# Kernel tuning notes

Measured on AMD Instinct MI355X. Metric: run time of the kernel, lower is better.

The kernel has to match this reference:

```python
import jax, jax.numpy as jnp
import numpy as np

# Static video grid (F, H, W); S = F*H*W tokens.
F_FRAMES, H_GRID, W_GRID = 9, 16, 28
DIM, N_HEADS = 1536, 12
HEAD_DIM = DIM // N_HEADS          # 128
ROT = HEAD_DIM // 2                # 64 complex pairs
EPS = 1e-6


def setup_inputs() -> dict:
    key = jax.random.key(0)
    ks = jax.random.split(key, 12)
    S = F_FRAMES * H_GRID * W_GRID
    scale = 0.02
    inp = {
        "x": jax.random.normal(ks[0], (1, S, DIM), jnp.float32),
        "seq_lens": jnp.array([S], jnp.int32),
        "grid_sizes": jnp.array([[F_FRAMES, H_GRID, W_GRID]], jnp.int32),
        "freqs": jax.random.normal(ks[1], (1024, ROT), jnp.float32),  # rope angles
        "Wq": jax.random.normal(ks[2], (DIM, DIM), jnp.float32) * scale,
        "bq": jnp.zeros((DIM,), jnp.float32),
        "Wk": jax.random.normal(ks[3], (DIM, DIM), jnp.float32) * scale,
        "bk": jnp.zeros((DIM,), jnp.float32),
        "Wv": jax.random.normal(ks[4], (DIM, DIM), jnp.float32) * scale,
        "bv": jnp.zeros((DIM,), jnp.float32),
        "Wo": jax.random.normal(ks[5], (DIM, DIM), jnp.float32) * scale,
        "bo": jnp.zeros((DIM,), jnp.float32),
        "gq": jnp.ones((DIM,), jnp.float32),
        "gk": jnp.ones((DIM,), jnp.float32),
    }
    return inp


def _rms_norm(h, g):
    # WanRMSNorm: h * rsqrt(mean(h^2) + eps) * weight
    var = jnp.mean(jnp.square(h), axis=-1, keepdims=True)
    return h * jax.lax.rsqrt(var + EPS) * g


def _rope_angles(freqs):
    # Split channel dim into temporal / height / width parts.
    c = ROT
    t_dim = c - 2 * (c // 3)  # 22
    s1 = c // 3               # 21
    temporal, height, width = freqs[:, :t_dim], freqs[:, t_dim:t_dim + s1], freqs[:, t_dim + s1:]
    t_ang = jnp.repeat(temporal[:F_FRAMES], H_GRID * W_GRID, axis=0)         # [S, 22]
    h_ang = jnp.tile(jnp.repeat(height[:H_GRID], W_GRID, axis=0), (F_FRAMES, 1))  # [S, 21]
    w_ang = jnp.tile(jnp.tile(width[:W_GRID], (H_GRID, 1)), (F_FRAMES, 1))        # [S, 21]
    return jnp.concatenate([t_ang, h_ang, w_ang], axis=-1)  # [S, c]


def _rope_apply(x, ang):
    # x: [B, S, n, d] viewed as complex pairs [B, S, n, d/2, 2]
    b, s, n, d = x.shape
    xp = x.reshape(b, s, n, d // 2, 2)
    xr, xi = xp[..., 0], xp[..., 1]
    cos = jnp.cos(ang)[None, :, None, :]
    sin = jnp.sin(ang)[None, :, None, :]
    out_r = xr * cos - xi * sin
    out_i = xr * sin + xi * cos
    return jnp.stack([out_r, out_i], axis=-1).reshape(b, s, n, d)


def reference(x, seq_lens, grid_sizes, freqs, Wq, bq, Wk, bk, Wv, bv, Wo, bo, gq, gk):
    b, s, _ = x.shape
    n, d = N_HEADS, HEAD_DIM
    q = _rms_norm(x @ Wq + bq, gq).reshape(b, s, n, d)
    k = _rms_norm(x @ Wk + bk, gk).reshape(b, s, n, d)
    v = (x @ Wv + bv).reshape(b, s, n, d)

    ang = _rope_angles(freqs)  # [S, d/2]
    rq = _rope_apply(q, ang)
    rk = _rope_apply(k, ang)

    # Causal frame-block mask: query in frame i attends to kv in frames <= i.
    frame_idx = jnp.arange(s) // (H_GRID * W_GRID)
    mask = frame_idx[None, :] <= frame_idx[:, None]  # [S_q, S_k]

    scale = 1.0 / jnp.sqrt(jnp.asarray(d, x.dtype))
    scores = jnp.einsum("bqnd,bknd->bnqk", rq, rk) * scale
    scores = jnp.where(mask[None, None], scores, jnp.asarray(-1e30, scores.dtype))
    probs = jax.nn.softmax(scores, axis=-1)
    attn = jnp.einsum("bnqk,bknd->bqnd", probs, v).reshape(b, s, n * d)
    return attn @ Wo + bo
```

## Files before the change

kernel.cpp:

```cpp
#include <hip/hip_runtime.h>
#include <stdint.h>

typedef unsigned short u16;
typedef unsigned int u32;
typedef __attribute__((ext_vector_type(8))) short bf16x8;
typedef __attribute__((ext_vector_type(4))) float f32x4;

#define S_LEN 4032
#define S_PAD 4096
#define DIMC  1536
#define HD    128
#define FRAME 448

static const size_t OFF_FLAG  = 0;
static const size_t OFF_CANON = 256;
static const size_t OFF_XB    = 524288;
static const size_t OFF_WT    = OFF_XB  + 12582912;
static const size_t OFF_WOT   = OFF_WT  + 14155776;
static const size_t OFF_YQ    = OFF_WOT + 4718592;
static const size_t OFF_YK    = OFF_YQ  + 12582912;
static const size_t OFF_VT    = OFF_YK  + 12582912;
static const size_t OFF_QH    = OFF_VT  + 12582912;
static const size_t OFF_KH    = OFF_QH  + 12386304;
static const size_t OFF_AT    = OFF_KH  + 12386304;
static const size_t WS_NEED   = OFF_AT  + 12582912;

#define C_BQ 0
#define C_BO 4608
#define C_GQ 6144
#define C_GK 7680
#define C_FR 9216
#define C_TOT 74752

__device__ __forceinline__ u16 f2bf(float f) {
  union { float f; u32 u; } v; v.f = f;
  u32 u = v.u;
  u32 r = (u + 0x7fffu + ((u >> 16) & 1u)) >> 16;
  return (u16)r;
}
__device__ __forceinline__ float bf2f(u16 h) {
  union { float f; u32 u; } v; v.u = ((u32)h) << 16;
  return v.f;
}

__device__ __forceinline__ void gld_lds16(const void* g, void* l) {
  __builtin_amdgcn_global_load_lds(
      (const __attribute__((address_space(1))) void*)(uintptr_t)g,
      (__attribute__((address_space(3))) void*)(u32)(uintptr_t)l,
      16, 0, 0);
}

__device__ __forceinline__ f32x4 mfma16(bf16x8 a, bf16x8 b, f32x4 c) {
  return __builtin_amdgcn_mfma_f32_16x16x32_bf16(a, b, c, 0, 0, 0);
}

__global__ void detect_dtype(const u16* __restrict__ x, int* __restrict__ flag) {
  __shared__ int cnt;
  if (threadIdx.x == 0) cnt = 0;
  __syncthreads();
  int e = (x[2 * threadIdx.x] >> 7) & 0xff;
  if (e > 150) atomicAdd(&cnt, 1);
  __syncthreads();
  if (threadIdx.x == 0) *flag = (cnt >= 8) ? 1 : 0;
}

__global__ void prep_small(const void* bq, const void* bk, const void* bv, const void* bo,
                           const void* gq, const void* gk, const void* fr,
                           float* __restrict__ canon, const int* __restrict__ flagp) {
  int fl = *flagp;
  for (int i = blockIdx.x * 256 + threadIdx.x; i < C_TOT; i += gridDim.x * 256) {
    const void* src; int j;
    if      (i < 1536) { src = bq; j = i; }
    else if (i < 3072) { src = bk; j = i - 1536; }
    else if (i < 4608) { src = bv; j = i - 3072; }
    else if (i < 6144) { src = bo; j = i - 4608; }
    else if (i < 7680) { src = gq; j = i - 6144; }
    else if (i < 9216) { src = gk; j = i - 7680; }
    else               { src = fr; j = i - 9216; }
    canon[i] = fl ? ((const float*)src)[j] : bf2f(((const u16*)src)[j]);
  }
}

__global__ void convert_x(const void* __restrict__ xin, u16* __restrict__ xb,
                          const int* __restrict__ flagp) {
  int fl = *flagp;
  int i = blockIdx.x * 256 + threadIdx.x;
  if (i >= (S_PAD * DIMC) / 8) return;
  size_t base = (size_t)i * 8;
  int row = (int)(base / DIMC);
  union { u16 h[8]; uint4 v; } u;
  if (row < S_LEN) {
    if (fl) {
      const float* xf = (const float*)xin + base;
      #pragma unroll
      for (int j = 0; j < 8; j++) u.h[j] = f2bf(xf[j]);
    } else {
      const u16* xh = (const u16*)xin + base;
      #pragma unroll
      for (int j = 0; j < 8; j++) u.h[j] = xh[j];
    }
  } else {
    #pragma unroll
    for (int j = 0; j < 8; j++) u.h[j] = 0;
  }
  ((uint4*)xb)[i] = u.v;
}

__global__ void transpose_w(const void* Wq, const void* Wk, const void* Wv, const void* Wo,
                            u16* __restrict__ wqkvt, u16* __restrict__ wot,
                            const int* __restrict__ flagp) {
  int fl = *flagp;
  int z = blockIdx.z;
  const void* W = (z == 0) ? Wq : (z == 1) ? Wk : (z == 2) ? Wv : Wo;
  u16* dst = (z < 3) ? (wqkvt + (size_t)z * DIMC * DIMC) : wot;
  __shared__ float tile[32][33];
  int tx = threadIdx.x, ty = threadIdx.y;
  int c = blockIdx.x * 32 + tx;
  #pragma unroll
  for (int i = 0; i < 4; i++) {
    int r = blockIdx.y * 32 + ty + i * 8;
    float v = fl ? ((const float*)W)[(size_t)r * DIMC + c]
                 : bf2f(((const u16*)W)[(size_t)r * DIMC + c]);
    tile[ty + i * 8][tx] = v;
  }
  __syncthreads();
  int k = blockIdx.y * 32 + tx;
  #pragma unroll
  for (int i = 0; i < 4; i++) {
    int n = blockIdx.x * 32 + ty + i * 8;
    dst[(size_t)n * DIMC + k] = f2bf(tile[tx][ty + i * 8]);
  }
}

template <int MODE, int NBN>
__launch_bounds__(256, 4)
__global__ void gemm_bt(const u16* __restrict__ A, const u16* __restrict__ Bt,
                        const float* __restrict__ canon,
                        u16* __restrict__ Yq, u16* __restrict__ Yk, u16* __restrict__ Vt,
                        void* __restrict__ Out, const int* __restrict__ flagp) {
  const int bid = blockIdx.x;
  const int panel = bid / (8 * NBN);
  const int rem = bid % (8 * NBN);
  const int bm0 = (panel * 8 + (rem % 8)) * 128;
  const int bn0 = (rem / 8) * 128;
  const int tid = threadIdx.x, wave = tid >> 6, lane = tid & 63;
  const int wm = wave >> 1, wn = wave & 1;
  const int l15 = lane & 15, l4 = lane >> 4;
  __shared__ u16 sA[128 * 64];
  __shared__ u16 sB[128 * 64];
  f32x4 acc[4][4];
  #pragma unroll
  for (int i = 0; i < 4; i++)
    #pragma unroll
    for (int j = 0; j < 4; j++) acc[i][j] = (f32x4){0.f, 0.f, 0.f, 0.f};

  const int swc = ((lane & 7) ^ (lane >> 3)) * 8;
  const u16* Ab = A  + (size_t)(bm0 + (lane >> 3)) * DIMC + swc;
  const u16* Bb = Bt + (size_t)(bn0 + (lane >> 3)) * DIMC + swc;

  for (int kt = 0; kt < DIMC; kt += 64) {
    __syncthreads();
    #pragma unroll
    for (int c = 0; c < 4; c++) {
      int g = wave * 4 + c;
      gld_lds16(Ab + (size_t)g * 8 * DIMC + kt, (char*)sA + g * 1024);
      gld_lds16(Bb + (size_t)g * 8 * DIMC + kt, (char*)sB + g * 1024);
    }
    __syncthreads();
    #pragma unroll
    for (int ks = 0; ks < 2; ks++) {
      bf16x8 av[4], bvv[4];
      #pragma unroll
      for (int mt = 0; mt < 4; mt++)
        av[mt]  = *(const bf16x8*)(sA + (wm * 64 + mt * 16 + l15) * 64 +
                                   (((ks * 4 + l4) ^ (l15 & 7)) * 8));
      #pragma unroll
      for (int nt = 0; nt < 4; nt++)
        bvv[nt] = *(const bf16x8*)(sB + (wn * 64 + nt * 16 + l15) * 64 +
                                   (((ks * 4 + l4) ^ (l15 & 7)) * 8));
      #pragma unroll
      for (int mt = 0; mt < 4; mt++)
        #pragma unroll
        for (int nt = 0; nt < 4; nt++)
          acc[mt][nt] = mfma16(av[mt], bvv[nt], acc[mt][nt]);
    }
  }

  const int gm0 = bm0 + wm * 64;
  const int gn0 = bn0 + wn * 64;
  if (MODE == 0) {
    #pragma unroll
    for (int nt = 0; nt < 4; nt++) {
      int gn = gn0 + nt * 16 + l15;
      float b = canon[C_BQ + gn];
      #pragma unroll
      for (int mt = 0; mt < 4; mt++) {
        int gm = gm0 + mt * 16 + l4 * 4;
        if (gn < 1536) {
          #pragma unroll
          for (int r = 0; r < 4; r++)
            Yq[(size_t)(gm + r) * DIMC + gn] = f2bf(acc[mt][nt][r] + b);
        } else if (gn < 3072) {
          int g2 = gn - 1536;
          #pragma unroll
          for (int r = 0; r < 4; r++)
            Yk[(size_t)(gm + r) * DIMC + g2] = f2bf(acc[mt][nt][r] + b);
        } else {
          int g2 = gn - 3072;
          u32 lo = (u32)f2bf(acc[mt][nt][0] + b) | ((u32)f2bf(acc[mt][nt][1] + b) << 16);
          u32 hi = (u32)f2bf(acc[mt][nt][2] + b) | ((u32)f2bf(acc[mt][nt][3] + b) << 16);
          uint2 pk; pk.x = lo; pk.y = hi;
          *(uint2*)(Vt + (size_t)g2 * S_PAD + gm) = pk;
        }
      }
    }
  } else {
    const int fl = *flagp;
    #pragma unroll
    for (int nt = 0; nt < 4; nt++) {
      int gn = gn0 + nt * 16 + l15;
      float b = canon[C_BO + gn];
      #pragma unroll
      for (int mt = 0; mt < 4; mt++) {
        int gm = gm0 + mt * 16 + l4 * 4;
        #pragma unroll
        for (int r = 0; r < 4; r++) {
          int gr = gm + r;
          if (gr < S_LEN) {
            float v = acc[mt][nt][r] + b;
            if (fl) ((float*)Out)[(size_t)gr * DIMC + gn] = v;
            else    ((u16*)Out)[(size_t)gr * DIMC + gn] = f2bf(v);
          }
        }
      }
    }
  }
}

__global__ void norm_rope(const u16* __restrict__ Yq, const u16* __restrict__ Yk,
                          const float* __restrict__ canon, u16* __restrict__ Qh,
                          u16* __restrict__ Kh) {
  const int tid = threadIdx.x, wave = tid >> 6, lane = tid & 63;
  const int s = blockIdx.x * 4 + wave;
  const int isq = (blockIdx.y == 0);
  const u16* Y = isq ? Yq : Yk;
  const float* g = canon + (isq ? C_GQ : C_GK);
  u16* Oh = isq ? Qh : Kh;
  const float sc = isq ? (0.08838834764831845f * 1.4426950408889634f) : 1.0f;

  const u32* yrow = (const u32*)Y + (size_t)s * 768;
  float xr[12], xi[12];
  float ss = 0.f;
  #pragma unroll
  for (int i = 0; i < 12; i++) {
    u32 d = yrow[lane + 64 * i];
    float a = bf2f((u16)(d & 0xffff));
    float b = bf2f((u16)(d >> 16));
    xr[i] = a; xi[i] = b;
    ss += a * a + b * b;
  }
  #pragma unroll
  for (int dd = 1; dd < 64; dd <<= 1) ss += __shfl_xor(ss, dd, 64);
  float rms = rsqrtf(ss * (1.f / 1536.f) + 1e-6f);

  int f_ = s / FRAME, hh = (s % FRAME) / 28, ww = s % 28;
  const float* fr = canon + C_FR;
  float a = (lane < 22) ? fr[f_ * 64 + lane]
          : (lane < 43) ? fr[hh * 64 + lane]
                        : fr[ww * 64 + lane];
  float si, co;
  __sincosf(a, &si, &co);

  const float2* g2 = (const float2*)g;
  #pragma unroll
  for (int i = 0; i < 12; i++) {
    int p = lane + 64 * i;
    float2 gg = g2[p];
    float r  = xr[i] * rms * gg.x;
    float im = xi[i] * rms * gg.y;
    u32 pk = (u32)f2bf((r * co - im * si) * sc) | ((u32)f2bf((r * si + im * co) * sc) << 16);
    ((u32*)Oh)[((size_t)i * S_LEN + s) * 64 + lane] = pk;
  }
}

__launch_bounds__(256, 2)
__global__ void attn_v5(const u16* __restrict__ Qh, const u16* __restrict__ Kh,
                        const u16* __restrict__ Vt, u16* __restrict__ Ab) {
  const int tid = threadIdx.x, wave = tid >> 6, lane = tid & 63;
  const int l15 = lane & 15, l4 = lane >> 4;
  const int pair = wave >> 1, m = wave & 1;
  const int h = blockIdx.x % 12;
  const int qb = 62 - (blockIdx.x / 12);
  const int q0 = qb * 64;
  const int nkv = (q0 / FRAME + 1) * 7;
  __shared__ u16 sK[2][8192];
  __shared__ u16 sV[2][8192];
  __shared__ u16 sP[8][1024];

  int koff[8], voff[8];
  #pragma unroll
  for (int i = 0; i < 8; i++) {
    int c = i * 128 + m * 64 + lane;
    int r = c >> 4, cc = (c & 15) ^ (r & 15);
    koff[i] = r * HD + cc * 8;
    int rv = c >> 3, cv = (c & 7) ^ (rv & 7);
    voff[i] = rv * S_PAD + cv * 8;
  }

  bf16x8 qf[4][2];
  #pragma unroll
  for (int ct = 0; ct < 2; ct++) {
    const u16* qp = Qh + ((size_t)h * S_LEN + q0 + m * 32 + ct * 16 + l15) * HD + l4 * 8;
    #pragma unroll
    for (int ks = 0; ks < 4; ks++) qf[ks][ct] = *(const bf16x8*)(qp + ks * 32);
  }
  f32x4 o[8][2];
  #pragma unroll
  for (int i = 0; i < 8; i++)
    #pragma unroll
    for (int ct = 0; ct < 2; ct++) o[i][ct] = (f32x4){0.f, 0.f, 0.f, 0.f};
  float l_i[2] = {0.f, 0.f};

  const u16* kb0 = Kh + (size_t)h * S_LEN * HD;
  const u16* vb0 = Vt + (size_t)h * HD * S_PAD;
  const int niter = (nkv + 1) >> 1;

  for (int it = 0; it < niter; ++it) {
    const int t = it * 2 + pair;
    const bool active = (t < nkv);
    __syncthreads();
    if (active) {
      const u16* kb = kb0 + (size_t)t * 64 * HD;
      const u16* vb = vb0 + t * 64;
      #pragma unroll
      for (int i = 0; i < 8; i++) {
        gld_lds16(kb + koff[i], (char*)sK[pair] + i * 2048 + m * 1024);
        gld_lds16(vb + voff[i], (char*)sV[pair] + i * 2048 + m * 1024);
      }
    }
    __syncthreads();
    if (!active) continue;

    f32x4 sT[4][2];
    #pragma unroll
    for (int nt = 0; nt < 4; nt++)
      #pragma unroll
      for (int ct = 0; ct < 2; ct++) sT[nt][ct] = (f32x4){0.f, 0.f, 0.f, 0.f};
    #pragma unroll
    for (int ks = 0; ks < 4; ks++) {
      bf16x8 kf[4];
      #pragma unroll
      for (int nt = 0; nt < 4; nt++)
        kf[nt] = *(const bf16x8*)(sK[pair] + (nt * 16 + l15) * HD + (((ks * 4 + l4) ^ l15) * 8));
      #pragma unroll
      for (int nt = 0; nt < 4; nt++)
        #pragma unroll
        for (int ct = 0; ct < 2; ct++)
          sT[nt][ct] = mfma16(kf[nt], qf[ks][ct], sT[nt][ct]);
    }

    #pragma unroll
    for (int ct = 0; ct < 2; ct++) {
      float rs = 0.f;
      #pragma unroll
      for (int nt = 0; nt < 4; nt++)
        #pragma unroll
        for (int r = 0; r < 4; r++) {
          float p = __builtin_amdgcn_exp2f(sT[nt][ct][r]);
          sT[nt][ct][r] = p; rs += p;
        }
      l_i[ct] += rs;
      u16* pw = sP[wave * 2 + ct];
      #pragma unroll
      for (int nt = 0; nt < 4; nt++) {
        u32 lo = (u32)f2bf(sT[nt][ct][0]) | ((u32)f2bf(sT[nt][ct][1]) << 16);
        u32 hi = (u32)f2bf(sT[nt][ct][2]) | ((u32)f2bf(sT[nt][ct][3]) << 16);
        u32 off = (u32)((nt >> 1) * 512 + ((nt & 1) * 2 + (l4 >> 1)) * 128 + l15 * 8 + (l4 & 1) * 4);
        uint2 pk; pk.x = lo; pk.y = hi;
        *(uint2*)(pw + off) = pk;
      }
    }

    #pragma unroll
    for (int ks2 = 0; ks2 < 2; ks2++) {
      bf16x8 pb[2];
      #pragma unroll
      for (int ct = 0; ct < 2; ct++)
        pb[ct] = *(const bf16x8*)(sP[wave * 2 + ct] + ks2 * 512 + lane * 8);
      #pragma unroll
      for (int vt = 0; vt < 8; vt++) {
        bf16x8 vf = *(const bf16x8*)(sV[pair] + (vt * 16 + l15) * 64 + (((ks2 * 4 + l4) ^ (l15 & 7)) * 8));
        #pragma unroll
        for (int ct = 0; ct < 2; ct++)
          o[vt][ct] = mfma16(vf, pb[ct], o[vt][ct]);
      }
    }
  }

  #pragma unroll
  for (int ct = 0; ct < 2; ct++) {
    l_i[ct] += __shfl_xor(l_i[ct], 16, 64);
    l_i[ct] += __shfl_xor(l_i[ct], 32, 64);
  }
  __syncthreads();
  float* mb = (float*)sK;
  float* lb = (float*)sP;
  if (pair == 1) {
    #pragma unroll
    for (int ct = 0; ct < 2; ct++) {
      #pragma unroll
      for (int vt = 0; vt < 8; vt++)
        *(f32x4*)(mb + m * 4096 + (ct * 8 + vt) * 256 + lane * 4) = o[vt][ct];
      lb[m * 128 + ct * 64 + lane] = l_i[ct];
    }
  }
  __syncthreads();
  if (pair == 0) {
    #pragma unroll
    for (int ct = 0; ct < 2; ct++) {
      float l = l_i[ct] + lb[m * 128 + ct * 64 + lane];
      float inv = 1.f / l;
      const size_t orow = (size_t)(q0 + m * 32 + ct * 16 + l15) * DIMC + (size_t)h * HD;
      #pragma unroll
      for (int vt = 0; vt < 8; vt++) {
        f32x4 op = *(const f32x4*)(mb + m * 4096 + (ct * 8 + vt) * 256 + lane * 4);
        float o0 = (o[vt][ct][0] + op[0]) * inv;
        float o1 = (o[vt][ct][1] + op[1]) * inv;
        float o2 = (o[vt][ct][2] + op[2]) * inv;
        float o3 = (o[vt][ct][3] + op[3]) * inv;
        u32 lo = (u32)f2bf(o0) | ((u32)f2bf(o1) << 16);
        u32 hi = (u32)f2bf(o2) | ((u32)f2bf(o3) << 16);
        uint2 pk; pk.x = lo; pk.y = hi;
        *(uint2*)(Ab + orow + vt * 16 + l4 * 4) = pk;
      }
    }
  }
}

extern "C" void kernel_launch(void* const* d_in, const int* in_sizes, int n_in,
                              void* d_out, int out_size, void* d_ws, size_t ws_size,
                              hipStream_t stream) {
  if (ws_size < WS_NEED) return;
  char* ws = (char*)d_ws;
  int*   flag  = (int*)(ws + OFF_FLAG);
  float* canon = (float*)(ws + OFF_CANON);
  u16* xb    = (u16*)(ws + OFF_XB);
  u16* wqkvt = (u16*)(ws + OFF_WT);
  u16* wot   = (u16*)(ws + OFF_WOT);
  u16* yq    = (u16*)(ws + OFF_YQ);
  u16* yk    = (u16*)(ws + OFF_YK);
  u16* vt    = (u16*)(ws + OFF_VT);
  u16* qh    = (u16*)(ws + OFF_QH);
  u16* kh    = (u16*)(ws + OFF_KH);
  u16* ab    = (u16*)(ws + OFF_AT);

  const void* x  = d_in[0];
  const void* fr = d_in[3];
  const void* Wq = d_in[4];  const void* bq = d_in[5];
  const void* Wk = d_in[6];  const void* bk = d_in[7];
  const void* Wv = d_in[8];  const void* bv = d_in[9];
  const void* Wo = d_in[10]; const void* bo = d_in[11];
  const void* gq = d_in[12]; const void* gk = d_in[13];

  detect_dtype<<<1, 256, 0, stream>>>((const u16*)x, flag);
  prep_small<<<292, 256, 0, stream>>>(bq, bk, bv, bo, gq, gk, fr, canon, flag);
  convert_x<<<3072, 256, 0, stream>>>(x, xb, flag);
  transpose_w<<<dim3(48, 48, 4), dim3(32, 8), 0, stream>>>(Wq, Wk, Wv, Wo, wqkvt, wot, flag);
  gemm_bt<0, 36><<<1152, 256, 0, stream>>>(xb, wqkvt, canon, yq, yk, vt, nullptr, flag);
  norm_rope<<<dim3(1008, 2), 256, 0, stream>>>(yq, yk, canon, qh, kh);
  attn_v5<<<756, 256, 0, stream>>>(qh, kh, vt, ab);
  gemm_bt<1, 12><<<384, 256, 0, stream>>>(ab, wot, canon, nullptr, nullptr, nullptr, d_out, flag);
}
```

Before: 339.1 us.

## Split each KV tile across wave pairs in attention and drop GEMM block swizzle

The attention kernel now loads one 64-key tile per iteration, shared by all four waves, with each wave pair handling 32 of the keys. The old scheme gave each wave pair its own tile. This halves shared memory (one K/V buffer and a smaller P buffer) and raises the launch-bounds occupancy hint from 2 to 3 blocks per SM, aiming to hide latency better. The cost is twice as many loop iterations, each with two barriers, and less MFMA work per barrier. Separately, the GEMMs replace the grouped panel block mapping with a plain 2D grid, which may reduce L2 reuse.

Result: slower. 361.7 us (+6.6%).

```diff
diff --git a/kernel.cpp b/kernel.cpp
--- a/kernel.cpp
+++ b/kernel.cpp
@@ -132,17 +132,13 @@
   }
 }
 
-template <int MODE, int NBN>
+template <int MODE>
 __launch_bounds__(256, 4)
 __global__ void gemm_bt(const u16* __restrict__ A, const u16* __restrict__ Bt,
                         const float* __restrict__ canon,
                         u16* __restrict__ Yq, u16* __restrict__ Yk, u16* __restrict__ Vt,
                         void* __restrict__ Out, const int* __restrict__ flagp) {
-  const int bid = blockIdx.x;
-  const int panel = bid / (8 * NBN);
-  const int rem = bid % (8 * NBN);
-  const int bm0 = (panel * 8 + (rem % 8)) * 128;
-  const int bn0 = (rem / 8) * 128;
+  const int bm0 = blockIdx.y * 128, bn0 = blockIdx.x * 128;
   const int tid = threadIdx.x, wave = tid >> 6, lane = tid & 63;
   const int wm = wave >> 1, wn = wave & 1;
   const int l15 = lane & 15, l4 = lane >> 4;
@@ -283,27 +279,28 @@
   }
 }
 
-__launch_bounds__(256, 2)
-__global__ void attn_v5(const u16* __restrict__ Qh, const u16* __restrict__ Kh,
+__launch_bounds__(256, 3)
+__global__ void attn_v6(const u16* __restrict__ Qh, const u16* __restrict__ Kh,
                         const u16* __restrict__ Vt, u16* __restrict__ Ab) {
   const int tid = threadIdx.x, wave = tid >> 6, lane = tid & 63;
   const int l15 = lane & 15, l4 = lane >> 4;
-  const int pair = wave >> 1, m = wave & 1;
+  const int kh = wave >> 1, m = wave & 1;
   const int h = blockIdx.x % 12;
   const int qb = 62 - (blockIdx.x / 12);
   const int q0 = qb * 64;
   const int nkv = (q0 / FRAME + 1) * 7;
-  __shared__ u16 sK[2][8192];
-  __shared__ u16 sV[2][8192];
-  __shared__ u16 sP[8][1024];
-
-  int koff[8], voff[8];
-  #pragma unroll
-  for (int i = 0; i < 8; i++) {
-    int c = i * 128 + m * 64 + lane;
-    int r = c >> 4, cc = (c & 15) ^ (r & 15);
-    koff[i] = r * HD + cc * 8;
-    int rv = c >> 3, cv = (c & 7) ^ (rv & 7);
+  __shared__ u16 sKV[16384];
+  __shared__ u16 sP[8][512];
+  u16* sK = sKV;
+  u16* sV = sKV + 8192;
+
+  int koff[4], voff[4];
+  #pragma unroll
+  for (int i = 0; i < 4; i++) {
+    int s = (wave * 4 + i) * 64 + lane;
+    int r = s >> 4, c = (s & 15) ^ (r & 15);
+    koff[i] = r * HD + c * 8;
+    int rv = s >> 3, cv = (s & 7) ^ (rv & 7);
     voff[i] = rv * S_PAD + cv * 8;
   }
 
@@ -323,37 +320,33 @@
 
   const u16* kb0 = Kh + (size_t)h * S_LEN * HD;
   const u16* vb0 = Vt + (size_t)h * HD * S_PAD;
-  const int niter = (nkv + 1) >> 1;
-
-  for (int it = 0; it < niter; ++it) {
-    const int t = it * 2 + pair;
-    const bool active = (t < nkv);
+
+  for (int t = 0; t < nkv; ++t) {
     __syncthreads();
-    if (active) {
+    {
       const u16* kb = kb0 + (size_t)t * 64 * HD;
       const u16* vb = vb0 + t * 64;
       #pragma unroll
-      for (int i = 0; i < 8; i++) {
-        gld_lds16(kb + koff[i], (char*)sK[pair] + i * 2048 + m * 1024);
-        gld_lds16(vb + voff[i], (char*)sV[pair] + i * 2048 + m * 1024);
+      for (int i = 0; i < 4; i++) {
+        gld_lds16(kb + koff[i], (char*)sK + (wave * 4 + i) * 1024);
+        gld_lds16(vb + voff[i], (char*)sV + (wave * 4 + i) * 1024);
       }
     }
     __syncthreads();
-    if (!active) continue;
-
-    f32x4 sT[4][2];
-    #pragma unroll
-    for (int nt = 0; nt < 4; nt++)
+
+    f32x4 sT[2][2];
+    #pragma unroll
+    for (int nt = 0; nt < 2; nt++)
       #pragma unroll
       for (int ct = 0; ct < 2; ct++) sT[nt][ct] = (f32x4){0.f, 0.f, 0.f, 0.f};
     #pragma unroll
     for (int ks = 0; ks < 4; ks++) {
-      bf16x8 kf[4];
-      #pragma unroll
-      for (int nt = 0; nt < 4; nt++)
-        kf[nt] = *(const bf16x8*)(sK[pair] + (nt * 16 + l15) * HD + (((ks * 4 + l4) ^ l15) * 8));
-      #pragma unroll
-      for (int nt = 0; nt < 4; nt++)
+      bf16x8 kf[2];
+      #pragma unroll
+      for (int nt = 0; nt < 2; nt++)
+        kf[nt] = *(const bf16x8*)(sK + (kh * 32 + nt * 16 + l15) * HD + (((ks * 4 + l4) ^ l15) * 8));
+      #pragma unroll
+      for (int nt = 0; nt < 2; nt++)
         #pragma unroll
         for (int ct = 0; ct < 2; ct++)
           sT[nt][ct] = mfma16(kf[nt], qf[ks][ct], sT[nt][ct]);
@@ -363,7 +356,7 @@
     for (int ct = 0; ct < 2; ct++) {
       float rs = 0.f;
       #pragma unroll
-      for (int nt = 0; nt < 4; nt++)
+      for (int nt = 0; nt < 2; nt++)
         #pragma unroll
         for (int r = 0; r < 4; r++) {
           float p = __builtin_amdgcn_exp2f(sT[nt][ct][r]);
@@ -372,28 +365,25 @@
       l_i[ct] += rs;
       u16* pw = sP[wave * 2 + ct];
       #pragma unroll
-      for (int nt = 0; nt < 4; nt++) {
+      for (int nt = 0; nt < 2; nt++) {
         u32 lo = (u32)f2bf(sT[nt][ct][0]) | ((u32)f2bf(sT[nt][ct][1]) << 16);
         u32 hi = (u32)f2bf(sT[nt][ct][2]) | ((u32)f2bf(sT[nt][ct][3]) << 16);
-        u32 off = (u32)((nt >> 1) * 512 + ((nt & 1) * 2 + (l4 >> 1)) * 128 + l15 * 8 + (l4 & 1) * 4);
+        u32 off = (u32)((nt * 2 + (l4 >> 1)) * 128 + l15 * 8 + (l4 & 1) * 4);
         uint2 pk; pk.x = lo; pk.y = hi;
         *(uint2*)(pw + off) = pk;
       }
     }
 
-    #pragma unroll
-    for (int ks2 = 0; ks2 < 2; ks2++) {
-      bf16x8 pb[2];
+    bf16x8 pb[2];
+    #pragma unroll
+    for (int ct = 0; ct < 2; ct++)
+      pb[ct] = *(const bf16x8*)(sP[wave * 2 + ct] + lane * 8);
+    #pragma unroll
+    for (int vt = 0; vt < 8; vt++) {
+      bf16x8 vf = *(const bf16x8*)(sV + (vt * 16 + l15) * 64 + (((kh * 4 + l4) ^ (l15 & 7)) * 8));
       #pragma unroll
       for (int ct = 0; ct < 2; ct++)
-        pb[ct] = *(const bf16x8*)(sP[wave * 2 + ct] + ks2 * 512 + lane * 8);
-      #pragma unroll
-      for (int vt = 0; vt < 8; vt++) {
-        bf16x8 vf = *(const bf16x8*)(sV[pair] + (vt * 16 + l15) * 64 + (((ks2 * 4 + l4) ^ (l15 & 7)) * 8));
-        #pragma unroll
-        for (int ct = 0; ct < 2; ct++)
-          o[vt][ct] = mfma16(vf, pb[ct], o[vt][ct]);
-      }
+        o[vt][ct] = mfma16(vf, pb[ct], o[vt][ct]);
     }
   }
 
@@ -403,27 +393,27 @@
     l_i[ct] += __shfl_xor(l_i[ct], 32, 64);
   }
   __syncthreads();
-  float* mb = (float*)sK;
+  float* mb = (float*)sKV;
   float* lb = (float*)sP;
-  if (pair == 1) {
+  if (kh == 1) {
     #pragma unroll
     for (int ct = 0; ct < 2; ct++) {
       #pragma unroll
       for (int vt = 0; vt < 8; vt++)
-        *(f32x4*)(mb + m * 4096 + (ct * 8 + vt) * 256 + lane * 4) = o[vt][ct];
-      lb[m * 128 + ct * 64 + lane] = l_i[ct];
+        *(f32x4*)(mb + ((((m * 2 + ct) * 8 + vt) * 64) + lane) * 4) = o[vt][ct];
+      lb[(m * 2 + ct) * 64 + lane] = l_i[ct];
     }
   }
   __syncthreads();
-  if (pair == 0) {
+  if (kh == 0) {
     #pragma unroll
     for (int ct = 0; ct < 2; ct++) {
-      float l = l_i[ct] + lb[m * 128 + ct * 64 + lane];
+      float l = l_i[ct] + lb[(m * 2 + ct) * 64 + lane];
       float inv = 1.f / l;
       const size_t orow = (size_t)(q0 + m * 32 + ct * 16 + l15) * DIMC + (size_t)h * HD;
       #pragma unroll
       for (int vt = 0; vt < 8; vt++) {
-        f32x4 op = *(const f32x4*)(mb + m * 4096 + (ct * 8 + vt) * 256 + lane * 4);
+        f32x4 op = *(const f32x4*)(mb + ((((m * 2 + ct) * 8 + vt) * 64) + lane) * 4);
         float o0 = (o[vt][ct][0] + op[0]) * inv;
         float o1 = (o[vt][ct][1] + op[1]) * inv;
         float o2 = (o[vt][ct][2] + op[2]) * inv;
@@ -466,8 +456,8 @@
   prep_small<<<292, 256, 0, stream>>>(bq, bk, bv, bo, gq, gk, fr, canon, flag);
   convert_x<<<3072, 256, 0, stream>>>(x, xb, flag);
   transpose_w<<<dim3(48, 48, 4), dim3(32, 8), 0, stream>>>(Wq, Wk, Wv, Wo, wqkvt, wot, flag);
-  gemm_bt<0, 36><<<1152, 256, 0, stream>>>(xb, wqkvt, canon, yq, yk, vt, nullptr, flag);
+  gemm_bt<0><<<dim3(36, 32), 256, 0, stream>>>(xb, wqkvt, canon, yq, yk, vt, nullptr, flag);
   norm_rope<<<dim3(1008, 2), 256, 0, stream>>>(yq, yk, canon, qh, kh);
-  attn_v5<<<756, 256, 0, stream>>>(qh, kh, vt, ab);
-  gemm_bt<1, 12><<<384, 256, 0, stream>>>(ab, wot, canon, nullptr, nullptr, nullptr, d_out, flag);
-}
+  attn_v6<<<756, 256, 0, stream>>>(qh, kh, vt, ab);
+  gemm_bt<1><<<dim3(12, 32), 256, 0, stream>>>(ab, wot, canon, nullptr, nullptr, nullptr, d_out, flag);
+}
```
